# Performance work log

Measured on AMD Instinct MI355X. Metric: run time of the kernel, lower is better.

Reference implementation:

```python
import jax, jax.numpy as jnp
import numpy as np

# Module config (from init_kwargs): Occ3D-nuScenes volume
VOL_MIN = np.array([-40.0, -40.0, -1.0], dtype=np.float32)
VOXEL_SIZE = 0.4
GRID_SHAPE = (200, 200, 16)  # (vol_max - vol_min) / voxel_size
K = 6          # fixed per-gaussian window; covers radii <= 0.6m (bbox span <= 5 voxels)
N_GAUSS = 32768
N_DIMS = 16


def setup_inputs() -> dict:
    key = jax.random.key(0)
    k1, k2, k3, k4, k5 = jax.random.split(key, 5)
    # Means strictly inside the volume with 1m margin so bboxes stay in-grid.
    lo = jnp.array([-39.0, -39.0, 0.0], dtype=jnp.float32)
    hi = jnp.array([39.0, 39.0, 4.4], dtype=jnp.float32)
    means3d = jax.random.uniform(k1, (N_GAUSS, 3), minval=lo, maxval=hi, dtype=jnp.float32)
    # SPD covariances: Q diag(s) Q^T with eigenvalues in [0.01, 0.04]
    A = jax.random.normal(k2, (N_GAUSS, 3, 3), dtype=jnp.float32)
    Q, _ = jnp.linalg.qr(A)
    s = jax.random.uniform(k3, (N_GAUSS, 3), minval=0.01, maxval=0.04, dtype=jnp.float32)
    covs = jnp.einsum('nij,nj,nkj->nik', Q, s, Q)
    opacities = jax.random.uniform(k4, (N_GAUSS,), dtype=jnp.float32)
    features = jax.random.normal(k5, (N_GAUSS, N_DIMS), dtype=jnp.float32)
    return {"means3d": means3d, "covs": covs, "opacities": opacities, "features": features}


def reference(means3d, covs, opacities, features):
    N, D = features.shape
    dim_x, dim_y, dim_z = GRID_SHAPE
    total = dim_x * dim_y * dim_z
    vol_min = jnp.asarray(VOL_MIN)

    inv_covs = jnp.linalg.inv(covs)                                  # [N,3,3]
    radii = 3.0 * jnp.sqrt(jnp.diagonal(covs, axis1=-2, axis2=-1))   # [N,3]

    # Bounding box in voxel indices (trunc toward zero, like the triton .to(int32))
    s = (means3d - radii - vol_min) / VOXEL_SIZE
    e = (means3d + radii - vol_min) / VOXEL_SIZE
    start = jnp.maximum(0, s.astype(jnp.int32))                      # [N,3]
    end = jnp.minimum(jnp.array(GRID_SHAPE, jnp.int32), e.astype(jnp.int32) + 1)

    offs = jnp.arange(K, dtype=jnp.int32)
    ix = start[:, 0:1] + offs   # [N,K]
    iy = start[:, 1:2] + offs
    iz = start[:, 2:3] + offs
    mask = ((ix < end[:, 0:1])[:, :, None, None]
            & (iy < end[:, 1:2])[:, None, :, None]
            & (iz < end[:, 2:3])[:, None, None, :])                  # [N,K,K,K]

    # Voxel-corner minus mean offsets (matches kernel: x*vs + vol_min - m)
    px = ix.astype(means3d.dtype) * VOXEL_SIZE + vol_min[0] - means3d[:, 0:1]  # [N,K]
    py = iy.astype(means3d.dtype) * VOXEL_SIZE + vol_min[1] - means3d[:, 1:2]
    pz = iz.astype(means3d.dtype) * VOXEL_SIZE + vol_min[2] - means3d[:, 2:3]
    d = jnp.stack(jnp.broadcast_arrays(px[:, :, None, None],
                                       py[:, None, :, None],
                                       pz[:, None, None, :]), axis=-1)  # [N,K,K,K,3]

    mahal = jnp.einsum('nxyzi,nij,nxyzj->nxyz', d, inv_covs, d)      # [N,K,K,K]
    density = opacities[:, None, None, None] * jnp.exp(-0.5 * mahal)
    density = jnp.where(mask, density, 0.0)

    flat_idx = (ix[:, :, None, None] * (dim_y * dim_z)
                + iy[:, None, :, None] * dim_z
                + iz[:, None, None, :])                               # [N,K,K,K]
    idx = flat_idx.reshape(-1)

    grid_density = jnp.zeros((total,), density.dtype).at[idx].add(density.reshape(-1))

    contrib = density[..., None] * features[:, None, None, None, :]   # [N,K,K,K,D]
    grid_feats = jnp.zeros((total, D), density.dtype).at[:, -1].set(1e-5)
    grid_feats = grid_feats.at[idx].add(contrib.reshape(-1, D))
    grid_feats = grid_feats / jnp.clip(grid_density, 1e-6, None)[:, None]

    return grid_density.reshape(GRID_SHAPE), grid_feats.reshape(*GRID_SHAPE, D)
```

## Files before the change

kernel.cpp:

```cpp
#include <hip/hip_runtime.h>
#include <math.h>

constexpr int   GX = 200, GY = 200, GZ = 16;
constexpr int   TOTAL = GX * GY * GZ;
constexpr int   ND = 16;
constexpr int   KW = 6;
constexpr float VS = 0.4f;
constexpr float VMINX = -40.0f, VMINY = -40.0f, VMINZ = -1.0f;

constexpr int   TS = 4;
constexpr int   TX = 50, TY = 50, TZ = 4;
constexpr int   NT = TX * TY * TZ;
constexpr int   RS = 20;
constexpr int   CAP = 128;
constexpr int   BR  = 12;
constexpr float NHL2E = -0.72134752044448170f;


__device__ __forceinline__ unsigned bf16_rne(float x) {
    unsigned u = __float_as_uint(x);
    return (u + 0x7fffu + ((u >> 16) & 1u)) >> 16;
}

__global__ __launch_bounds__(256) void gv_prep(
    const float* __restrict__ means, const float* __restrict__ covs,
    const float* __restrict__ opac,  const float* __restrict__ feats,
    float* __restrict__ gdata, int* __restrict__ counts,
    int* __restrict__ entries, int n)
{
    int g = blockIdx.x * 256 + threadIdx.x;
    if (g >= n) return;
    const float* cv = covs + (size_t)g * 9;
    float a = cv[0], b = cv[1], c = cv[2], d = cv[4], e = cv[5], f = cv[8];
    float A = d * f - e * e;
    float B = c * e - b * f;
    float C = b * e - c * d;
    float invdet = 1.0f / (a * A + b * B + c * C);
    float mx = means[g * 3 + 0], my = means[g * 3 + 1], mz = means[g * 3 + 2];
    float rx = 3.0f * sqrtf(a), ry = 3.0f * sqrtf(d), rz = 3.0f * sqrtf(f);
    int sx = max(0, (int)((mx - rx - VMINX) / VS));
    int sy = max(0, (int)((my - ry - VMINY) / VS));
    int sz = max(0, (int)((mz - rz - VMINZ) / VS));
    int ex = min(GX, (int)((mx + rx - VMINX) / VS) + 1); ex = min(ex, sx + KW);
    int ey = min(GY, (int)((my + ry - VMINY) / VS) + 1); ey = min(ey, sy + KW);
    int ez = min(GZ, (int)((mz + rz - VMINZ) / VS) + 1); ez = min(ez, sz + KW);

    float rec[RS];
    rec[0] = mx; rec[1] = my; rec[2] = mz; rec[3] = opac[g];
    rec[4] = (A * invdet) * NHL2E;
    rec[5] = (B * invdet) * (2.0f * NHL2E);
    rec[6] = (C * invdet) * (2.0f * NHL2E);
    rec[7] = ((a * f - c * c) * invdet) * NHL2E;
    rec[8] = ((b * c - a * e) * invdet) * (2.0f * NHL2E);
    rec[9] = ((a * d - b * b) * invdet) * NHL2E;
    rec[10] = __int_as_float(sx | (sy << 8) | (sz << 16));
    rec[11] = __int_as_float(ex | (ey << 8) | (ez << 16));
    const float* fr = feats + (size_t)g * ND;
#pragma unroll
    for (int q = 0; q < 8; ++q) {
        unsigned lo = bf16_rne(fr[2 * q]);
        unsigned hi = bf16_rne(fr[2 * q + 1]);
        rec[12 + q] = __uint_as_float(lo | (hi << 16));
    }
    float4* dst = (float4*)(gdata + (size_t)g * RS);
#pragma unroll
    for (int q = 0; q < 5; ++q) dst[q] = ((const float4*)rec)[q];

    int tx0 = sx >> 2, tx1 = (ex - 1) >> 2;
    int ty0 = sy >> 2, ty1 = (ey - 1) >> 2;
    int tz0 = sz >> 2, tz1 = (ez - 1) >> 2;
    for (int tx = tx0; tx <= tx1; ++tx)
        for (int ty = ty0; ty <= ty1; ++ty)
            for (int tz = tz0; tz <= tz1; ++tz) {
                int tile = (tx * TY + ty) * TZ + tz;
                int slot = atomicAdd(&counts[tile], 1);
                if (slot < CAP) entries[(size_t)tile * CAP + slot] = g;
            }
}

__global__ __launch_bounds__(256) void gv_tile(
    const float* __restrict__ gdata, const int* __restrict__ counts,
    const int* __restrict__ entries, float* __restrict__ out)
{
    const int wv   = threadIdx.x >> 6;
    const int lane = threadIdx.x & 63;
    const int p    = blockIdx.x * 4 + wv;
    const int tz   = p % TZ;
    const int ty   = (p / TZ) % TY;
    const int tx   = p / (TZ * TY);

    __shared__ float sbuf[4][2][BR * RS];

    const int lz = lane & 3, ly = (lane >> 2) & 3, lx = lane >> 4;
    const int ix = tx * TS + lx, iy = ty * TS + ly, iz = tz * TS + lz;
    const float pxc = (float)ix * VS + VMINX;
    const float pyc = (float)iy * VS + VMINY;
    const float pzc = (float)iz * VS + VMINZ;

    float accd = 0.0f;
    float accf[ND];
#pragma unroll
    for (int c = 0; c < ND; ++c) accf[c] = 0.0f;
    accf[ND - 1] = 1e-5f;

    const int cnt = __builtin_amdgcn_readfirstlane(min(counts[p], CAP));
    const int* __restrict__ el = entries + (size_t)p * CAP;

    const int  rl = lane / 5;
    const int  fc = lane - rl * 5;
    const bool stager = lane < 60;
    const int  wslot = rl * RS + fc * 4;

    if (cnt > 0) {
        const int nb = (cnt + BR - 1) / BR;
        float* b0 = &sbuf[wv][0][0];
        float* b1 = &sbuf[wv][1][0];

        float4 vn; int idn2 = 0;
        if (stager) {
            int id0 = el[min(rl, cnt - 1)];
            float4 v0 = *(const float4*)(gdata + (size_t)id0 * RS + fc * 4);
            *(float4*)(b0 + wslot) = v0;
            int idn = el[min(BR + rl, cnt - 1)];
            vn = *(const float4*)(gdata + (size_t)idn * RS + fc * 4);
            idn2 = el[min(2 * BR + rl, cnt - 1)];
        }

        for (int b = 0; b < nb; ++b) {
            if (b + 1 < nb && stager) {
                float* dstb = ((b + 1) & 1) ? b1 : b0;
                *(float4*)(dstb + wslot) = vn;
                vn = *(const float4*)(gdata + (size_t)idn2 * RS + fc * 4);
                idn2 = el[min((b + 3) * BR + rl, cnt - 1)];
            }
            const float* rb = (b & 1) ? b1 : b0;
            const int rn = min(BR, cnt - b * BR);
            for (int r = 0; r < rn; ++r) {
                const float* rec = rb + r * RS;
                float4 c2 = *(const float4*)(rec + 8);
                int spk = __float_as_int(c2.z), epk = __float_as_int(c2.w);
                int sx = spk & 255, sy = (spk >> 8) & 255, sz = (spk >> 16) & 255;
                int ex = epk & 255, ey = (epk >> 8) & 255, ez = (epk >> 16) & 255;
                bool in = (ix >= sx) & (ix < ex)
                        & (iy >= sy) & (iy < ey)
                        & (iz >= sz) & (iz < ez);

                float4 c0 = *(const float4*)(rec);
                float4 c1 = *(const float4*)(rec + 4);
                float px = pxc - c0.x;
                float py = pyc - c0.y;
                float pz = pzc - c0.z;
                float q = c1.x * px * px + c1.w * py * py + c2.y * pz * pz
                        + c1.y * px * py + c1.z * px * pz + c2.x * py * pz;
                float dens = c0.w * __builtin_amdgcn_exp2f(q);
                dens = in ? dens : 0.0f;
                accd += dens;

                uint4 fA = *(const uint4*)(rec + 12);
                uint4 fB = *(const uint4*)(rec + 16);
#define BFLO(u) __uint_as_float((u) << 16)
#define BFHI(u) __uint_as_float((u) & 0xffff0000u)
                accf[0]  = fmaf(dens, BFLO(fA.x), accf[0]);
                accf[1]  = fmaf(dens, BFHI(fA.x), accf[1]);
                accf[2]  = fmaf(dens, BFLO(fA.y), accf[2]);
                accf[3]  = fmaf(dens, BFHI(fA.y), accf[3]);
                accf[4]  = fmaf(dens, BFLO(fA.z), accf[4]);
                accf[5]  = fmaf(dens, BFHI(fA.z), accf[5]);
                accf[6]  = fmaf(dens, BFLO(fA.w), accf[6]);
                accf[7]  = fmaf(dens, BFHI(fA.w), accf[7]);
                accf[8]  = fmaf(dens, BFLO(fB.x), accf[8]);
                accf[9]  = fmaf(dens, BFHI(fB.x), accf[9]);
                accf[10] = fmaf(dens, BFLO(fB.y), accf[10]);
                accf[11] = fmaf(dens, BFHI(fB.y), accf[11]);
                accf[12] = fmaf(dens, BFLO(fB.z), accf[12]);
                accf[13] = fmaf(dens, BFHI(fB.z), accf[13]);
                accf[14] = fmaf(dens, BFLO(fB.w), accf[14]);
                accf[15] = fmaf(dens, BFHI(fB.w), accf[15]);
#undef BFLO
#undef BFHI
            }
        }
    }

    const int flat = (ix * GY + iy) * GZ + iz;
    out[flat] = accd;
    float inv = 1.0f / fmaxf(accd, 1e-6f);
    float4* fo = (float4*)(out + TOTAL + (size_t)flat * ND);
#pragma unroll
    for (int q = 0; q < 4; ++q) {
        float4 w;
        w.x = accf[q * 4 + 0] * inv;
        w.y = accf[q * 4 + 1] * inv;
        w.z = accf[q * 4 + 2] * inv;
        w.w = accf[q * 4 + 3] * inv;
        fo[q] = w;
    }
}

extern "C" void kernel_launch(void* const* d_in, const int* in_sizes, int n_in,
                              void* d_out, int out_size, void* d_ws, size_t ws_size,
                              hipStream_t stream) {
    const float* means = (const float*)d_in[0];
    const float* covs  = (const float*)d_in[1];
    const float* opac  = (const float*)d_in[2];
    const float* feats = (const float*)d_in[3];
    float* out = (float*)d_out;
    const int n = in_sizes[2];

    float* gdata   = (float*)d_ws;
    int*   counts  = (int*)(gdata + (size_t)n * RS);
    int*   entries = counts + ((NT + 63) & ~63);

    hipMemsetAsync(counts, 0, NT * sizeof(int), stream);
    gv_prep<<<(n + 255) / 256, 256, 0, stream>>>(means, covs, opac, feats,
                                                 gdata, counts, entries, n);
    gv_tile<<<NT / 4, 256, 0, stream>>>(gdata, counts, entries, out);
}
```

Baseline: 106.7 us.

## Replace LDS double-buffered record staging with per-wave uniform register prefetch

Gaussian records are no longer staged cooperatively into LDS with a double-buffered ring. Each wave now loads the whole 20-float record with wave-uniform loads (tile index made uniform via readfirstlane) and software-prefetches the next record into registers, removing the LDS traffic and the staging logic. The prep kernel also drops to 64-thread blocks. The trade-off is higher register pressure and memory latency per gaussian that is hidden only one record deep.

```diff
diff --git a/kernel.cpp b/kernel.cpp
--- a/kernel.cpp
+++ b/kernel.cpp
@@ -13,7 +13,6 @@
 constexpr int   NT = TX * TY * TZ;
 constexpr int   RS = 20;
 constexpr int   CAP = 128;
-constexpr int   BR  = 12;
 constexpr float NHL2E = -0.72134752044448170f;
 
 
@@ -22,13 +21,13 @@
     return (u + 0x7fffu + ((u >> 16) & 1u)) >> 16;
 }
 
-__global__ __launch_bounds__(256) void gv_prep(
+__global__ __launch_bounds__(64) void gv_prep(
     const float* __restrict__ means, const float* __restrict__ covs,
     const float* __restrict__ opac,  const float* __restrict__ feats,
     float* __restrict__ gdata, int* __restrict__ counts,
     int* __restrict__ entries, int n)
 {
-    int g = blockIdx.x * 256 + threadIdx.x;
+    int g = blockIdx.x * 64 + threadIdx.x;
     if (g >= n) return;
     const float* cv = covs + (size_t)g * 9;
     float a = cv[0], b = cv[1], c = cv[2], d = cv[4], e = cv[5], f = cv[8];
@@ -78,18 +77,40 @@
             }
 }
 
+struct RecS {
+    float mx, my, mz, op;
+    float q00, q01, q02, q11;
+    float q12, q22;
+    unsigned spk, epk;
+    unsigned f0, f1, f2, f3, f4, f5, f6, f7;
+};
+
+__device__ __forceinline__ RecS load_rec(const float* __restrict__ rp) {
+    RecS c;
+    const float4 a = ((const float4*)rp)[0];
+    const float4 b = ((const float4*)rp)[1];
+    const float4 d = ((const float4*)rp)[2];
+    const uint4  e = ((const uint4*)rp)[3];
+    const uint4  f = ((const uint4*)rp)[4];
+    c.mx = a.x;  c.my = a.y;  c.mz = a.z;  c.op = a.w;
+    c.q00 = b.x; c.q01 = b.y; c.q02 = b.z; c.q11 = b.w;
+    c.q12 = d.x; c.q22 = d.y;
+    c.spk = __float_as_uint(d.z); c.epk = __float_as_uint(d.w);
+    c.f0 = e.x; c.f1 = e.y; c.f2 = e.z; c.f3 = e.w;
+    c.f4 = f.x; c.f5 = f.y; c.f6 = f.z; c.f7 = f.w;
+    return c;
+}
+
 __global__ __launch_bounds__(256) void gv_tile(
     const float* __restrict__ gdata, const int* __restrict__ counts,
     const int* __restrict__ entries, float* __restrict__ out)
 {
     const int wv   = threadIdx.x >> 6;
     const int lane = threadIdx.x & 63;
-    const int p    = blockIdx.x * 4 + wv;
+    const int p    = __builtin_amdgcn_readfirstlane(blockIdx.x * 4 + wv);
     const int tz   = p % TZ;
     const int ty   = (p / TZ) % TY;
     const int tx   = p / (TZ * TY);
-
-    __shared__ float sbuf[4][2][BR * RS];
 
     const int lz = lane & 3, ly = (lane >> 2) & 3, lx = lane >> 4;
     const int ix = tx * TS + lx, iy = ty * TS + ly, iz = tz * TS + lz;
@@ -103,82 +124,50 @@
     for (int c = 0; c < ND; ++c) accf[c] = 0.0f;
     accf[ND - 1] = 1e-5f;
 
-    const int cnt = __builtin_amdgcn_readfirstlane(min(counts[p], CAP));
+    const int cnt = min(counts[p], CAP);
     const int* __restrict__ el = entries + (size_t)p * CAP;
 
-    const int  rl = lane / 5;
-    const int  fc = lane - rl * 5;
-    const bool stager = lane < 60;
-    const int  wslot = rl * RS + fc * 4;
-
     if (cnt > 0) {
-        const int nb = (cnt + BR - 1) / BR;
-        float* b0 = &sbuf[wv][0][0];
-        float* b1 = &sbuf[wv][1][0];
-
-        float4 vn; int idn2 = 0;
-        if (stager) {
-            int id0 = el[min(rl, cnt - 1)];
-            float4 v0 = *(const float4*)(gdata + (size_t)id0 * RS + fc * 4);
-            *(float4*)(b0 + wslot) = v0;
-            int idn = el[min(BR + rl, cnt - 1)];
-            vn = *(const float4*)(gdata + (size_t)idn * RS + fc * 4);
-            idn2 = el[min(2 * BR + rl, cnt - 1)];
-        }
-
-        for (int b = 0; b < nb; ++b) {
-            if (b + 1 < nb && stager) {
-                float* dstb = ((b + 1) & 1) ? b1 : b0;
-                *(float4*)(dstb + wslot) = vn;
-                vn = *(const float4*)(gdata + (size_t)idn2 * RS + fc * 4);
-                idn2 = el[min((b + 3) * BR + rl, cnt - 1)];
-            }
-            const float* rb = (b & 1) ? b1 : b0;
-            const int rn = min(BR, cnt - b * BR);
-            for (int r = 0; r < rn; ++r) {
-                const float* rec = rb + r * RS;
-                float4 c2 = *(const float4*)(rec + 8);
-                int spk = __float_as_int(c2.z), epk = __float_as_int(c2.w);
-                int sx = spk & 255, sy = (spk >> 8) & 255, sz = (spk >> 16) & 255;
-                int ex = epk & 255, ey = (epk >> 8) & 255, ez = (epk >> 16) & 255;
-                bool in = (ix >= sx) & (ix < ex)
-                        & (iy >= sy) & (iy < ey)
-                        & (iz >= sz) & (iz < ez);
-
-                float4 c0 = *(const float4*)(rec);
-                float4 c1 = *(const float4*)(rec + 4);
-                float px = pxc - c0.x;
-                float py = pyc - c0.y;
-                float pz = pzc - c0.z;
-                float q = c1.x * px * px + c1.w * py * py + c2.y * pz * pz
-                        + c1.y * px * py + c1.z * px * pz + c2.x * py * pz;
-                float dens = c0.w * __builtin_amdgcn_exp2f(q);
-                dens = in ? dens : 0.0f;
-                accd += dens;
-
-                uint4 fA = *(const uint4*)(rec + 12);
-                uint4 fB = *(const uint4*)(rec + 16);
-#define BFLO(u) __uint_as_float((u) << 16)
-#define BFHI(u) __uint_as_float((u) & 0xffff0000u)
-                accf[0]  = fmaf(dens, BFLO(fA.x), accf[0]);
-                accf[1]  = fmaf(dens, BFHI(fA.x), accf[1]);
-                accf[2]  = fmaf(dens, BFLO(fA.y), accf[2]);
-                accf[3]  = fmaf(dens, BFHI(fA.y), accf[3]);
-                accf[4]  = fmaf(dens, BFLO(fA.z), accf[4]);
-                accf[5]  = fmaf(dens, BFHI(fA.z), accf[5]);
-                accf[6]  = fmaf(dens, BFLO(fA.w), accf[6]);
-                accf[7]  = fmaf(dens, BFHI(fA.w), accf[7]);
-                accf[8]  = fmaf(dens, BFLO(fB.x), accf[8]);
-                accf[9]  = fmaf(dens, BFHI(fB.x), accf[9]);
-                accf[10] = fmaf(dens, BFLO(fB.y), accf[10]);
-                accf[11] = fmaf(dens, BFHI(fB.y), accf[11]);
-                accf[12] = fmaf(dens, BFLO(fB.z), accf[12]);
-                accf[13] = fmaf(dens, BFHI(fB.z), accf[13]);
-                accf[14] = fmaf(dens, BFLO(fB.w), accf[14]);
-                accf[15] = fmaf(dens, BFHI(fB.w), accf[15]);
-#undef BFLO
-#undef BFHI
-            }
+        int id0 = el[0];
+        RecS cur = load_rec(gdata + (size_t)id0 * RS);
+        int idn = el[cnt > 1 ? 1 : 0];
+        for (int r = 0; r < cnt; ++r) {
+            RecS nxt = load_rec(gdata + (size_t)idn * RS);
+            idn = el[min(r + 2, cnt - 1)];
+
+            int sx = cur.spk & 255, sy = (cur.spk >> 8) & 255, sz = (cur.spk >> 16) & 255;
+            int ex = cur.epk & 255, ey = (cur.epk >> 8) & 255, ez = (cur.epk >> 16) & 255;
+            bool in = ((unsigned)(ix - sx) < (unsigned)(ex - sx))
+                    & ((unsigned)(iy - sy) < (unsigned)(ey - sy))
+                    & ((unsigned)(iz - sz) < (unsigned)(ez - sz));
+
+            float px = pxc - cur.mx;
+            float py = pyc - cur.my;
+            float pz = pzc - cur.mz;
+            float q = cur.q00 * px * px + cur.q11 * py * py + cur.q22 * pz * pz
+                    + cur.q01 * px * py + cur.q02 * px * pz + cur.q12 * py * pz;
+            float dens = cur.op * __builtin_amdgcn_exp2f(q);
+            dens = in ? dens : 0.0f;
+            accd += dens;
+
+            accf[0]  = fmaf(dens, __uint_as_float(cur.f0 << 16),         accf[0]);
+            accf[1]  = fmaf(dens, __uint_as_float(cur.f0 & 0xffff0000u), accf[1]);
+            accf[2]  = fmaf(dens, __uint_as_float(cur.f1 << 16),         accf[2]);
+            accf[3]  = fmaf(dens, __uint_as_float(cur.f1 & 0xffff0000u), accf[3]);
+            accf[4]  = fmaf(dens, __uint_as_float(cur.f2 << 16),         accf[4]);
+            accf[5]  = fmaf(dens, __uint_as_float(cur.f2 & 0xffff0000u), accf[5]);
+            accf[6]  = fmaf(dens, __uint_as_float(cur.f3 << 16),         accf[6]);
+            accf[7]  = fmaf(dens, __uint_as_float(cur.f3 & 0xffff0000u), accf[7]);
+            accf[8]  = fmaf(dens, __uint_as_float(cur.f4 << 16),         accf[8]);
+            accf[9]  = fmaf(dens, __uint_as_float(cur.f4 & 0xffff0000u), accf[9]);
+            accf[10] = fmaf(dens, __uint_as_float(cur.f5 << 16),         accf[10]);
+            accf[11] = fmaf(dens, __uint_as_float(cur.f5 & 0xffff0000u), accf[11]);
+            accf[12] = fmaf(dens, __uint_as_float(cur.f6 << 16),         accf[12]);
+            accf[13] = fmaf(dens, __uint_as_float(cur.f6 & 0xffff0000u), accf[13]);
+            accf[14] = fmaf(dens, __uint_as_float(cur.f7 << 16),         accf[14]);
+            accf[15] = fmaf(dens, __uint_as_float(cur.f7 & 0xffff0000u), accf[15]);
+
+            cur = nxt;
         }
     }
 
@@ -212,7 +201,7 @@
     int*   entries = counts + ((NT + 63) & ~63);
 
     hipMemsetAsync(counts, 0, NT * sizeof(int), stream);
-    gv_prep<<<(n + 255) / 256, 256, 0, stream>>>(means, covs, opac, feats,
-                                                 gdata, counts, entries, n);
+    gv_prep<<<(n + 63) / 64, 64, 0, stream>>>(means, covs, opac, feats,
+                                              gdata, counts, entries, n);
     gv_tile<<<NT / 4, 256, 0, stream>>>(gdata, counts, entries, out);
 }
```

Result: slower. 109.4 us (+2.5%).

## Split gaussian prep into record kernel and parallel 8-way tile binning kernel

Applied to the files above, without the earlier changes.

Separates record construction from tile binning into two kernels. The binning kernel assigns one thread per (gaussian, tile-corner) pair, at most 8 tiles since each bbox spans at most 2 tiles per axis, which replaces the serial per-gaussian nested loop of atomics. The record kernel now uses 64-thread blocks to spread work across more CUs. This adds an extra kernel launch and a re-read of the packed bbox from global memory.

```diff
diff --git a/kernel.cpp b/kernel.cpp
--- a/kernel.cpp
+++ b/kernel.cpp
@@ -22,13 +22,12 @@
     return (u + 0x7fffu + ((u >> 16) & 1u)) >> 16;
 }
 
-__global__ __launch_bounds__(256) void gv_prep(
+__global__ __launch_bounds__(64) void gv_rec(
     const float* __restrict__ means, const float* __restrict__ covs,
     const float* __restrict__ opac,  const float* __restrict__ feats,
-    float* __restrict__ gdata, int* __restrict__ counts,
-    int* __restrict__ entries, int n)
+    float* __restrict__ gdata, int n)
 {
-    int g = blockIdx.x * 256 + threadIdx.x;
+    int g = blockIdx.x * 64 + threadIdx.x;
     if (g >= n) return;
     const float* cv = covs + (size_t)g * 9;
     float a = cv[0], b = cv[1], c = cv[2], d = cv[4], e = cv[5], f = cv[8];
@@ -65,17 +64,32 @@
     float4* dst = (float4*)(gdata + (size_t)g * RS);
 #pragma unroll
     for (int q = 0; q < 5; ++q) dst[q] = ((const float4*)rec)[q];
-
-    int tx0 = sx >> 2, tx1 = (ex - 1) >> 2;
-    int ty0 = sy >> 2, ty1 = (ey - 1) >> 2;
-    int tz0 = sz >> 2, tz1 = (ez - 1) >> 2;
-    for (int tx = tx0; tx <= tx1; ++tx)
-        for (int ty = ty0; ty <= ty1; ++ty)
-            for (int tz = tz0; tz <= tz1; ++tz) {
-                int tile = (tx * TY + ty) * TZ + tz;
-                int slot = atomicAdd(&counts[tile], 1);
-                if (slot < CAP) entries[(size_t)tile * CAP + slot] = g;
-            }
+}
+
+__global__ __launch_bounds__(256) void gv_bin(
+    const float* __restrict__ gdata, int* __restrict__ counts,
+    int* __restrict__ entries, int n)
+{
+    int gid = blockIdx.x * 256 + threadIdx.x;
+    int g = gid >> 3;
+    if (g >= n) return;
+    int c = gid & 7;
+    int dx = c & 1, dy = (c >> 1) & 1, dz = (c >> 2) & 1;
+
+    const float2 se = *(const float2*)(gdata + (size_t)g * RS + 10);
+    int spk = __float_as_int(se.x), epk = __float_as_int(se.y);
+    int sx = spk & 255, sy = (spk >> 8) & 255, sz = (spk >> 16) & 255;
+    int ex = epk & 255, ey = (epk >> 8) & 255, ez = (epk >> 16) & 255;
+
+    int tx0 = sx >> 2, nx = ((ex - 1) >> 2) - tx0;
+    int ty0 = sy >> 2, ny = ((ey - 1) >> 2) - ty0;
+    int tz0 = sz >> 2, nz = ((ez - 1) >> 2) - tz0;
+
+    if (dx <= nx && dy <= ny && dz <= nz) {
+        int tile = ((tx0 + dx) * TY + (ty0 + dy)) * TZ + (tz0 + dz);
+        int slot = atomicAdd(&counts[tile], 1);
+        if (slot < CAP) entries[(size_t)tile * CAP + slot] = g;
+    }
 }
 
 __global__ __launch_bounds__(256) void gv_tile(
@@ -212,7 +226,7 @@
     int*   entries = counts + ((NT + 63) & ~63);
 
     hipMemsetAsync(counts, 0, NT * sizeof(int), stream);
-    gv_prep<<<(n + 255) / 256, 256, 0, stream>>>(means, covs, opac, feats,
-                                                 gdata, counts, entries, n);
+    gv_rec<<<(n + 63) / 64, 64, 0, stream>>>(means, covs, opac, feats, gdata, n);
+    gv_bin<<<(n * 8 + 255) / 256, 256, 0, stream>>>(gdata, counts, entries, n);
     gv_tile<<<NT / 4, 256, 0, stream>>>(gdata, counts, entries, out);
 }
```

Result: faster. 103.5 us (-3.0%).
